# Performance work log

Hardware: AMD Instinct MI355X
Metric: run time of the kernel (lower is better)

The kernel has to match this reference:

```python
import jax, jax.numpy as jnp
import numpy as np

UP = jnp.array([0.0, 1.0, 0.0], dtype=jnp.float32)
LEASH = 15.0


def q_inv(q):
    return jnp.concatenate([-q[..., :3], q[..., 3:]], axis=-1)


def q_mul(q1, q2):
    x1, y1, z1, w1 = q1[..., 0], q1[..., 1], q1[..., 2], q1[..., 3]
    x2, y2, z2, w2 = q2[..., 0], q2[..., 1], q2[..., 2], q2[..., 3]
    return jnp.stack([
        w1 * x2 + x1 * w2 + y1 * z2 - z1 * y2,
        w1 * y2 - x1 * z2 + y1 * w2 + z1 * x2,
        w1 * z2 + x1 * y2 - y1 * x2 + z1 * w2,
        w1 * w2 - x1 * x2 - y1 * y2 - z1 * z2], axis=-1)


def q_rot(q, v):
    qv, qw = q[..., :3], q[..., 3:]
    t = 2.0 * jnp.cross(qv, v)
    return v + qw * t + jnp.cross(qv, t)


def mat_to_quat(R):
    # Batched [E,3,3] -> [E,4] (x,y,z,w), matching the torch branch structure.
    r = lambda i, j: R[:, i, j]
    eps = 1e-12
    tr = r(0, 0) + r(1, 1) + r(2, 2)
    Sa = jnp.sqrt(jnp.maximum(tr + 1.0, eps)) * 2.0
    qa = jnp.stack([(r(2, 1) - r(1, 2)) / Sa, (r(0, 2) - r(2, 0)) / Sa,
                    (r(1, 0) - r(0, 1)) / Sa, 0.25 * Sa], -1)
    Sb = jnp.sqrt(jnp.maximum(1.0 + r(0, 0) - r(1, 1) - r(2, 2), eps)) * 2.0
    qb = jnp.stack([0.25 * Sb, (r(0, 1) + r(1, 0)) / Sb,
                    (r(0, 2) + r(2, 0)) / Sb, (r(2, 1) - r(1, 2)) / Sb], -1)
    Sc = jnp.sqrt(jnp.maximum(1.0 + r(1, 1) - r(0, 0) - r(2, 2), eps)) * 2.0
    qc = jnp.stack([(r(0, 1) + r(1, 0)) / Sc, 0.25 * Sc,
                    (r(1, 2) + r(2, 1)) / Sc, (r(0, 2) - r(2, 0)) / Sc], -1)
    Sd = jnp.sqrt(jnp.maximum(1.0 + r(2, 2) - r(0, 0) - r(1, 1), eps)) * 2.0
    qd = jnp.stack([(r(0, 2) + r(2, 0)) / Sd, (r(1, 2) + r(2, 1)) / Sd,
                    0.25 * Sd, (r(1, 0) - r(0, 1)) / Sd], -1)
    cond_b = ((r(0, 0) > r(1, 1)) & (r(0, 0) > r(2, 2)))[:, None]
    cond_c = (r(1, 1) > r(2, 2))[:, None]
    return jnp.where((tr > 0)[:, None], qa,
                     jnp.where(cond_b, qb, jnp.where(cond_c, qc, qd)))


def sfm_pose_loss(pred_t, pred_q, gt_t, gt_q, batch_counts):
    E = batch_counts.shape[0]
    N = pred_t.shape[0]
    counts = batch_counts.astype(jnp.float32)  # [E]
    seg = jnp.repeat(jnp.arange(E), batch_counts, total_repeat_length=N)  # [N]
    starts = jnp.cumsum(batch_counts) - batch_counts  # first index of each episode
    sseg = lambda x: jax.ops.segment_sum(x, seg, num_segments=E)

    # --- per-episode centering ---
    mu_p = sseg(pred_t) / counts[:, None]
    mu_g = sseg(gt_t) / counts[:, None]
    p_c = pred_t - mu_p[seg]
    g_c = gt_t - mu_g[seg]

    # degenerate episodes: too short or near-zero gt variance (unbiased var)
    g_var = sseg(jnp.sum(g_c ** 2, -1)) / (counts - 1.0)
    deg = (batch_counts < 4) | (g_var < 1e-4)  # [E]

    # --- Umeyama: batched 3x3 SVD of H = p_c^T @ g_c per episode ---
    H = sseg(p_c[:, :, None] * g_c[:, None, :])  # [E,3,3]
    H_safe = jnp.where(deg[:, None, None], jnp.diag(jnp.array([3.0, 2.0, 1.0])), H)
    U, S, Vh = jnp.linalg.svd(H_safe, full_matrices=False)
    V = jnp.swapaxes(Vh, -1, -2)
    R0 = jnp.einsum('eij,ekj->eik', V, U)  # V @ U^T
    sgn = jnp.where(jnp.linalg.det(R0) < 0, -1.0, 1.0)
    V_adj = V * jnp.stack([jnp.ones_like(sgn), jnp.ones_like(sgn), sgn], -1)[:, None, :]
    R = jnp.einsum('eij,ekj->eik', V_adj, U)  # [E,3,3]

    p_rot = jnp.einsum('nij,nj->ni', R[seg], p_c)
    denom = sseg(jnp.sum(p_c ** 2, -1))
    nom = sseg(jnp.sum(p_rot * g_c, -1))
    s = jnp.where(denom > 1e-6,
                  jnp.clip(nom / jnp.maximum(denom, 1e-6), 1e-3, 1e3), 1.0)

    # --- translation loss (per-episode mse, then mean over episodes) ---
    p_al = jnp.where(deg[seg][:, None], p_c, p_rot * s[seg][:, None])
    diff = p_al - g_c
    loss_trans = jnp.mean(sseg(jnp.sum(diff ** 2, -1)) / (counts * 3.0))

    # --- scale loss (only non-degenerate episodes) ---
    loss_scale = jnp.sum(jnp.where(deg, 0.0, jnp.log(jnp.abs(s) + 1e-6) ** 2)) / E

    # --- rotation loss ---
    q_align = mat_to_quat(R)  # [E,4]
    q0_p = pred_q[starts]
    q0_g = gt_q[starts]
    pq_deg = q_mul(q_inv(q0_p)[seg], pred_q)
    gq_deg = q_mul(q_inv(q0_g)[seg], gt_q)
    pq_ume = q_mul(q_align[seg], pred_q)
    dm = deg[seg][:, None]
    pq_al = jnp.where(dm, pq_deg, pq_ume)
    gq_al = jnp.where(dm, gq_deg, gt_q)
    dot = jnp.sum(pq_al * gq_al, -1)
    loss_rot = jnp.mean(sseg(1.0 - dot ** 2) / counts)

    # --- gravity loss ---
    up = jnp.broadcast_to(UP, pred_q.shape[:-1] + (3,))
    pu = q_rot(q_inv(pred_q), up)
    gu = q_rot(q_inv(gt_q), up)
    cos = jnp.sum(pu * gu, -1) / jnp.maximum(
        jnp.linalg.norm(pu, axis=-1) * jnp.linalg.norm(gu, axis=-1), 1e-8)
    loss_grav = jnp.mean(sseg(1.0 - cos) / counts)

    # --- frame0 leash (deadzone on first translation of each episode) ---
    mag = jnp.linalg.norm(pred_t[starts], axis=-1)
    loss_leash = jnp.mean(jnp.maximum(mag - LEASH, 0.0) ** 2)

    return jnp.stack([loss_trans, loss_rot, loss_grav, loss_leash, loss_scale])


def setup_inputs() -> dict:
    rng = np.random.default_rng(0)
    E = 4096
    counts = rng.integers(64, 449, size=E)
    counts[:8] = np.array([2, 3, 3, 2, 3, 2, 3, 3])  # exercise degenerate branch
    N = int(counts.sum())
    key = jax.random.key(0)
    k1, k2, k3, k4 = jax.random.split(key, 4)
    pred_t = jax.random.normal(k1, (N, 3), dtype=jnp.float32) * 5.0
    gt_t = jax.random.normal(k2, (N, 3), dtype=jnp.float32) * 5.0

    def rand_unit_quat(k):
        q = jax.random.normal(k, (N, 4), dtype=jnp.float32)
        return q / jnp.linalg.norm(q, axis=-1, keepdims=True)

    return {
        'pred_t': pred_t,
        'pred_q': rand_unit_quat(k3),
        'gt_t': gt_t,
        'gt_q': rand_unit_quat(k4),
        'batch_counts': jnp.asarray(counts, dtype=jnp.int32),
    }


def reference(pred_t, pred_q, gt_t, gt_q, batch_counts):
    # Returns [loss_trans, loss_rot, loss_grav, loss_leash, loss_scale]
    return sfm_pose_loss(pred_t, pred_q, gt_t, gt_q, batch_counts)
```

## Files before the change

kernel.cpp:

```cpp
#include <hip/hip_runtime.h>
#include <math.h>

__global__ void scan_kernel(const int* __restrict__ counts,
                            int* __restrict__ starts,
                            float* __restrict__ out, int E) {
    __shared__ int lds[1024];
    int tid = threadIdx.x;
    if (tid < 5) out[tid] = 0.0f;
    int base = tid * 4;
    int c0 = (base + 0 < E) ? counts[base + 0] : 0;
    int c1 = (base + 1 < E) ? counts[base + 1] : 0;
    int c2 = (base + 2 < E) ? counts[base + 2] : 0;
    int c3 = (base + 3 < E) ? counts[base + 3] : 0;
    lds[tid] = c0 + c1 + c2 + c3;
    __syncthreads();
    for (int off = 1; off < 1024; off <<= 1) {
        int v = lds[tid];
        int a = (tid >= off) ? lds[tid - off] : 0;
        __syncthreads();
        lds[tid] = v + a;
        __syncthreads();
    }
    int excl = (tid > 0) ? lds[tid - 1] : 0;
    if (base + 0 < E) starts[base + 0] = excl; excl += c0;
    if (base + 1 < E) starts[base + 1] = excl; excl += c1;
    if (base + 2 < E) starts[base + 2] = excl; excl += c2;
    if (base + 3 < E) starts[base + 3] = excl;
}

__device__ __forceinline__ float4 qmul4(float4 a, float4 b) {
    return make_float4(
        a.w*b.x + a.x*b.w + a.y*b.z - a.z*b.y,
        a.w*b.y - a.x*b.z + a.y*b.w + a.z*b.x,
        a.w*b.z + a.x*b.y - a.y*b.x + a.z*b.w,
        a.w*b.w - a.x*b.x - a.y*b.y - a.z*b.z);
}

__device__ __forceinline__ void qinv_rot_up(float4 q, float out[3]) {
    float qx = -q.x, qy = -q.y, qz = -q.z, qw = q.w;
    float tx = -2.f*qz;
    float ty = 0.f;
    float tz = 2.f*qx;
    out[0] = 0.f + qw*tx + (qy*tz - qz*ty);
    out[1] = 1.f + qw*ty + (qz*tx - qx*tz);
    out[2] = 0.f + qw*tz + (qx*ty - qy*tx);
}

__device__ __forceinline__ float wave_sum(float v) {
    v += __shfl_xor(v, 32);
    v += __shfl_xor(v, 16);
    v += __shfl_xor(v, 8);
    v += __shfl_xor(v, 4);
    v += __shfl_xor(v, 2);
    v += __shfl_xor(v, 1);
    return v;
}

#define NS 29
#define CHUNK 128
#define NCH 4

__device__ __forceinline__ void accum_point(
    int i, int ci, int start,
    const float* __restrict__ pred_t, const float4* __restrict__ pred_q,
    const float* __restrict__ gt_t,   const float4* __restrict__ gt_q,
    bool small_c, float4 q0pi, float4 q0gi, float acc[NS])
{
    int m = start + min(i, ci - 1);
    float px = pred_t[3*m+0], py = pred_t[3*m+1], pz = pred_t[3*m+2];
    float gx = gt_t[3*m+0],  gy = gt_t[3*m+1],  gz = gt_t[3*m+2];
    float4 pq = pred_q[m];
    float4 gq = gt_q[m];
    if (i < ci) {
        acc[0] += px; acc[1] += py; acc[2] += pz;
        acc[3] += gx; acc[4] += gy; acc[5] += gz;
        acc[6] += px*px + py*py + pz*pz;
        acc[7] += gx*gx + gy*gy + gz*gz;
        acc[8]  += px*gx; acc[9]  += px*gy; acc[10] += px*gz;
        acc[11] += py*gx; acc[12] += py*gy; acc[13] += py*gz;
        acc[14] += pz*gx; acc[15] += pz*gy; acc[16] += pz*gz;

        float mx =  pq.w*gq.x - pq.z*gq.y + pq.y*gq.z - pq.x*gq.w;
        float my =  pq.z*gq.x + pq.w*gq.y - pq.x*gq.z - pq.y*gq.w;
        float mz = -pq.y*gq.x + pq.x*gq.y + pq.w*gq.z - pq.z*gq.w;
        float mw =  pq.x*gq.x + pq.y*gq.y + pq.z*gq.z + pq.w*gq.w;
        acc[17] += mx*mx; acc[18] += mx*my; acc[19] += mx*mz; acc[20] += mx*mw;
        acc[21] += my*my; acc[22] += my*mz; acc[23] += my*mw;
        acc[24] += mz*mz; acc[25] += mz*mw; acc[26] += mw*mw;

        float pu[3], gu[3];
        qinv_rot_up(pq, pu);
        qinv_rot_up(gq, gu);
        float cosv = pu[0]*gu[0] + pu[1]*gu[1] + pu[2]*gu[2];
        acc[27] += 1.f - cosv;

        if (small_c) {
            float4 aa = qmul4(q0pi, pq);
            float4 bb = qmul4(q0gi, gq);
            float dd = aa.x*bb.x + aa.y*bb.y + aa.z*bb.z + aa.w*bb.w;
            acc[28] += 1.f - dd*dd;
        }
    }
}

__global__ __launch_bounds__(256) void pass1_kernel(
    const float* __restrict__ pred_t, const float4* __restrict__ pred_q,
    const float* __restrict__ gt_t,   const float4* __restrict__ gt_q,
    const int* __restrict__ counts, const int* __restrict__ starts,
    float* __restrict__ P, int E)
{
    int wv = threadIdx.x >> 6;
    int lane = threadIdx.x & 63;
    int e = blockIdx.x * 4 + wv;
    if (e >= E) return;
    int ci = counts[e];
    int ch = blockIdx.y;
    int base0 = ch * CHUNK;
    if (base0 >= ci) return;
    int start = starts[e];
    bool small_c = (ci < 4);
    float4 q0pi = make_float4(0.f,0.f,0.f,0.f), q0gi = q0pi;
    if (small_c) {
        float4 q0p = pred_q[start];
        float4 q0g = gt_q[start];
        q0pi = make_float4(-q0p.x, -q0p.y, -q0p.z, q0p.w);
        q0gi = make_float4(-q0g.x, -q0g.y, -q0g.z, q0g.w);
    }

    float acc[NS];
    #pragma unroll
    for (int k = 0; k < NS; ++k) acc[k] = 0.f;

    for (int base = base0; base < ci; base += NCH * CHUNK) {
        accum_point(base + lane,      ci, start, pred_t, pred_q, gt_t, gt_q,
                    small_c, q0pi, q0gi, acc);
        accum_point(base + 64 + lane, ci, start, pred_t, pred_q, gt_t, gt_q,
                    small_c, q0pi, q0gi, acc);
    }

    #pragma unroll
    for (int k = 0; k < NS; ++k) acc[k] = wave_sum(acc[k]);

    float outv = 0.f;
    #pragma unroll
    for (int k = 0; k < NS; ++k)
        if (lane == k) outv = acc[k];
    if (lane < 32)
        P[((size_t)ch * E + e) * 32 + lane] = outv;
}

__device__ void jacobi3f(float A[3][3], float V[3][3]) {
    V[0][0]=1.f; V[0][1]=0.f; V[0][2]=0.f;
    V[1][0]=0.f; V[1][1]=1.f; V[1][2]=0.f;
    V[2][0]=0.f; V[2][1]=0.f; V[2][2]=1.f;
    for (int sweep = 0; sweep < 6; ++sweep) {
        float off = A[0][1]*A[0][1] + A[0][2]*A[0][2] + A[1][2]*A[1][2];
        float dia = A[0][0]*A[0][0] + A[1][1]*A[1][1] + A[2][2]*A[2][2];
        if (off <= 1e-12f * (dia + 1e-30f)) break;
        for (int p = 0; p < 2; ++p) for (int q = p + 1; q < 3; ++q) {
            float apq = A[p][q];
            if (fabsf(apq) < 1e-30f) continue;
            float theta = (A[q][q] - A[p][p]) / (2.0f * apq);
            float t = ((theta >= 0.f) ? 1.f : -1.f) / (fabsf(theta) + sqrtf(theta*theta + 1.f));
            float cc = 1.f / sqrtf(t*t + 1.f);
            float ss = t * cc;
            float app = A[p][p], aqq = A[q][q];
            A[p][p] = app - t * apq;
            A[q][q] = aqq + t * apq;
            A[p][q] = 0.f; A[q][p] = 0.f;
            int r = 3 - p - q;
            float arp = A[r][p], arq = A[r][q];
            A[r][p] = cc*arp - ss*arq; A[p][r] = A[r][p];
            A[r][q] = ss*arp + cc*arq; A[q][r] = A[r][q];
            for (int i = 0; i < 3; ++i) {
                float vip = V[i][p], viq = V[i][q];
                V[i][p] = cc*vip - ss*viq;
                V[i][q] = ss*vip + cc*viq;
            }
        }
    }
}

__device__ void mat2quatf(const float R[3][3], float q[4]) {
    const float eps = 1e-12f;
    float tr = R[0][0] + R[1][1] + R[2][2];
    if (tr > 0.f) {
        float S = sqrtf(fmaxf(tr + 1.f, eps)) * 2.f;
        q[0] = (R[2][1]-R[1][2])/S; q[1] = (R[0][2]-R[2][0])/S;
        q[2] = (R[1][0]-R[0][1])/S; q[3] = 0.25f*S;
    } else if ((R[0][0] > R[1][1]) && (R[0][0] > R[2][2])) {
        float S = sqrtf(fmaxf(1.f + R[0][0] - R[1][1] - R[2][2], eps)) * 2.f;
        q[0] = 0.25f*S; q[1] = (R[0][1]+R[1][0])/S;
        q[2] = (R[0][2]+R[2][0])/S; q[3] = (R[2][1]-R[1][2])/S;
    } else if (R[1][1] > R[2][2]) {
        float S = sqrtf(fmaxf(1.f + R[1][1] - R[0][0] - R[2][2], eps)) * 2.f;
        q[0] = (R[0][1]+R[1][0])/S; q[1] = 0.25f*S;
        q[2] = (R[1][2]+R[2][1])/S; q[3] = (R[0][2]-R[2][0])/S;
    } else {
        float S = sqrtf(fmaxf(1.f + R[2][2] - R[0][0] - R[1][1], eps)) * 2.f;
        q[0] = (R[0][2]+R[2][0])/S; q[1] = (R[1][2]+R[2][1])/S;
        q[2] = 0.25f*S; q[3] = (R[1][0]-R[0][1])/S;
    }
}

__global__ __launch_bounds__(64) void finalize_kernel(
    const float* __restrict__ P, const int* __restrict__ counts,
    const int* __restrict__ starts, const float* __restrict__ pred_t,
    const float4* __restrict__ pred_q, const float4* __restrict__ gt_q,
    float* __restrict__ out, int E)
{
    int e = blockIdx.x * 64 + threadIdx.x;
    float v_trans = 0.f, v_rot = 0.f, v_grav = 0.f, v_leash = 0.f, v_scale = 0.f;
    if (e < E) {
        int ci = counts[e];
        int start = starts[e];
        float A[32];
        #pragma unroll
        for (int k = 0; k < 32; ++k) A[k] = 0.f;
        #pragma unroll
        for (int ch = 0; ch < NCH; ++ch) {
            if (ch * CHUNK < ci) {
                const float4* rp = (const float4*)(P + ((size_t)ch * E + e) * 32);
                #pragma unroll
                for (int j = 0; j < 8; ++j) {
                    float4 v = rp[j];
                    A[4*j+0] += v.x; A[4*j+1] += v.y;
                    A[4*j+2] += v.z; A[4*j+3] += v.w;
                }
            }
        }
        float c = (float)ci;
        float mu_p[3] = { A[0]/c, A[1]/c, A[2]/c };
        float mu_g[3] = { A[3]/c, A[4]/c, A[5]/c };
        float pp_c = A[6] - c*(mu_p[0]*mu_p[0]+mu_p[1]*mu_p[1]+mu_p[2]*mu_p[2]);
        float gg_c = A[7] - c*(mu_g[0]*mu_g[0]+mu_g[1]*mu_g[1]+mu_g[2]*mu_g[2]);
        float H[3][3];
        H[0][0]=A[8] -c*mu_p[0]*mu_g[0]; H[0][1]=A[9] -c*mu_p[0]*mu_g[1]; H[0][2]=A[10]-c*mu_p[0]*mu_g[2];
        H[1][0]=A[11]-c*mu_p[1]*mu_g[0]; H[1][1]=A[12]-c*mu_p[1]*mu_g[1]; H[1][2]=A[13]-c*mu_p[1]*mu_g[2];
        H[2][0]=A[14]-c*mu_p[2]*mu_g[0]; H[2][1]=A[15]-c*mu_p[2]*mu_g[1]; H[2][2]=A[16]-c*mu_p[2]*mu_g[2];
        float g_var = gg_c / (c - 1.0f);
        bool small_c = (ci < 4);
        bool deg = small_c || (g_var < 1e-4f);
        float trans, rot, scale = 0.f;
        if (deg) {
            float s28;
            if (small_c) {
                s28 = A[28];
            } else {
                float4 q0p = pred_q[start];
                float4 q0g = gt_q[start];
                float4 q0pi = make_float4(-q0p.x, -q0p.y, -q0p.z, q0p.w);
                float4 q0gi = make_float4(-q0g.x, -q0g.y, -q0g.z, q0g.w);
                float local = 0.f;
                for (int ii = 0; ii < ci; ++ii) {
                    float4 aa = qmul4(q0pi, pred_q[start + ii]);
                    float4 bb = qmul4(q0gi, gt_q[start + ii]);
                    float dd = aa.x*bb.x + aa.y*bb.y + aa.z*bb.z + aa.w*bb.w;
                    local += 1.f - dd*dd;
                }
                s28 = local;
            }
            float trH = H[0][0] + H[1][1] + H[2][2];
            trans = (pp_c - 2.f*trH + gg_c) / (c * 3.f);
            rot = s28 / c;
        } else {
            float B[3][3], V[3][3];
            for (int i = 0; i < 3; ++i)
                for (int j = 0; j < 3; ++j)
                    B[i][j] = H[0][i]*H[0][j] + H[1][i]*H[1][j] + H[2][i]*H[2][j];
            jacobi3f(B, V);
            float lam[3] = { B[0][0], B[1][1], B[2][2] };
            int idx[3] = {0, 1, 2};
            if (lam[idx[0]] < lam[idx[1]]) { int t = idx[0]; idx[0] = idx[1]; idx[1] = t; }
            if (lam[idx[0]] < lam[idx[2]]) { int t = idx[0]; idx[0] = idx[2]; idx[2] = t; }
            if (lam[idx[1]] < lam[idx[2]]) { int t = idx[1]; idx[1] = idx[2]; idx[2] = t; }
            float v1[3], v2[3], v3[3];
            for (int i = 0; i < 3; ++i) { v1[i] = V[i][idx[0]]; v2[i] = V[i][idx[1]]; v3[i] = V[i][idx[2]]; }
            float detV = v1[0]*(v2[1]*v3[2]-v2[2]*v3[1])
                       - v1[1]*(v2[0]*v3[2]-v2[2]*v3[0])
                       + v1[2]*(v2[0]*v3[1]-v2[1]*v3[0]);
            float sgnV = (detV < 0.f) ? -1.f : 1.f;
            float u1[3], u2[3], u3[3];
            for (int i = 0; i < 3; ++i) u1[i] = H[i][0]*v1[0] + H[i][1]*v1[1] + H[i][2]*v1[2];
            float n1 = fmaxf(sqrtf(u1[0]*u1[0]+u1[1]*u1[1]+u1[2]*u1[2]), 1e-30f);
            for (int i = 0; i < 3; ++i) u1[i] /= n1;
            for (int i = 0; i < 3; ++i) u2[i] = H[i][0]*v2[0] + H[i][1]*v2[1] + H[i][2]*v2[2];
            float d12 = u1[0]*u2[0]+u1[1]*u2[1]+u1[2]*u2[2];
            for (int i = 0; i < 3; ++i) u2[i] -= d12*u1[i];
            float n2 = fmaxf(sqrtf(u2[0]*u2[0]+u2[1]*u2[1]+u2[2]*u2[2]), 1e-30f);
            for (int i = 0; i < 3; ++i) u2[i] /= n2;
            u3[0] = u1[1]*u2[2] - u1[2]*u2[1];
            u3[1] = u1[2]*u2[0] - u1[0]*u2[2];
            u3[2] = u1[0]*u2[1] - u1[1]*u2[0];
            float R[3][3];
            for (int i = 0; i < 3; ++i)
                for (int k = 0; k < 3; ++k)
                    R[i][k] = v1[i]*u1[k] + v2[i]*u2[k] + sgnV*v3[i]*u3[k];
            float nom = 0.f;
            for (int k = 0; k < 3; ++k)
                for (int j = 0; j < 3; ++j)
                    nom += R[k][j] * H[j][k];
            float denom = pp_c;
            float s = 1.f;
            if (denom > 1e-6f) {
                s = nom / fmaxf(denom, 1e-6f);
                s = fminf(fmaxf(s, 1e-3f), 1e3f);
            }
            trans = (s*s*denom - 2.f*s*nom + gg_c) / (c * 3.f);
            float ls = logf(fabsf(s) + 1e-6f);
            scale = ls * ls;
            float q[4];
            mat2quatf(R, q);
            float quad = q[0]*q[0]*A[17] + q[1]*q[1]*A[21] + q[2]*q[2]*A[24] + q[3]*q[3]*A[26]
                + 2.f*(q[0]*q[1]*A[18] + q[0]*q[2]*A[19] + q[0]*q[3]*A[20]
                     + q[1]*q[2]*A[22] + q[1]*q[3]*A[23] + q[2]*q[3]*A[25]);
            rot = (c - quad) / c;
        }
        float grav = A[27] / c;
        float tx = pred_t[3*start+0], ty = pred_t[3*start+1], tz = pred_t[3*start+2];
        float mag = sqrtf(tx*tx + ty*ty + tz*tz);
        float ml = fmaxf(mag - 15.f, 0.f);
        float Ed = (float)E;
        v_trans = trans / Ed;
        v_rot   = rot / Ed;
        v_grav  = grav / Ed;
        v_leash = (ml * ml) / Ed;
        v_scale = scale / Ed;
    }
    float vals[5] = { v_trans, v_rot, v_grav, v_leash, v_scale };
    #pragma unroll
    for (int k = 0; k < 5; ++k) {
        float v = wave_sum(vals[k]);
        if (threadIdx.x == 0) atomicAdd(out + k, v);
    }
}

extern "C" void kernel_launch(void* const* d_in, const int* in_sizes, int n_in,
                              void* d_out, int out_size, void* d_ws, size_t ws_size,
                              hipStream_t stream) {
    const float*  pred_t = (const float*)d_in[0];
    const float4* pred_q = (const float4*)d_in[1];
    const float*  gt_t   = (const float*)d_in[2];
    const float4* gt_q   = (const float4*)d_in[3];
    const int*    counts = (const int*)d_in[4];
    int E = in_sizes[4];

    int* starts = (int*)d_ws;
    size_t off = ((size_t)E * sizeof(int) + 255) & ~(size_t)255;
    float* P = (float*)((char*)d_ws + off);

    scan_kernel<<<1, 1024, 0, stream>>>(counts, starts, (float*)d_out, E);
    dim3 g1((E + 3) / 4, NCH);
    pass1_kernel<<<g1, 256, 0, stream>>>(pred_t, pred_q, gt_t, gt_q,
                                         counts, starts, P, E);
    finalize_kernel<<<(E + 63) / 64, 64, 0, stream>>>(P, counts, starts, pred_t,
                                                      pred_q, gt_q, (float*)d_out, E);
}
```

Baseline: 129.7 us.

## Use shuffle-based scan and two waves per episode with four points per lane

The block scan now uses wave shuffle prefix sums plus a small cross-wave pass instead of a barrier-heavy 1024-step LDS scan. Pass1 changes from four 128-point chunks per episode over a 2D grid to two waves per episode, each covering 256 contiguous points with four consecutive points per lane, and all loads are issued before the accumulation. The finalize step now sums two partials per episode instead of four. This aims to cut barrier cost, raise memory-level parallelism and halve the partial traffic. The price is less coalesced strided access per lane and fewer waves per episode.

```diff
diff --git a/kernel.cpp b/kernel.cpp
--- a/kernel.cpp
+++ b/kernel.cpp
@@ -1,27 +1,42 @@
 #include <hip/hip_runtime.h>
 #include <math.h>
+
+#define NS 29
+#define WPTS 256
 
 __global__ void scan_kernel(const int* __restrict__ counts,
                             int* __restrict__ starts,
                             float* __restrict__ out, int E) {
-    __shared__ int lds[1024];
+    __shared__ int wtot[16];
     int tid = threadIdx.x;
+    int lane = tid & 63, wv = tid >> 6;
     if (tid < 5) out[tid] = 0.0f;
     int base = tid * 4;
     int c0 = (base + 0 < E) ? counts[base + 0] : 0;
     int c1 = (base + 1 < E) ? counts[base + 1] : 0;
     int c2 = (base + 2 < E) ? counts[base + 2] : 0;
     int c3 = (base + 3 < E) ? counts[base + 3] : 0;
-    lds[tid] = c0 + c1 + c2 + c3;
+    int s = c0 + c1 + c2 + c3;
+    int incl = s;
+    #pragma unroll
+    for (int d = 1; d < 64; d <<= 1) {
+        int t = __shfl_up(incl, d);
+        if (lane >= d) incl += t;
+    }
+    if (lane == 63) wtot[wv] = incl;
     __syncthreads();
-    for (int off = 1; off < 1024; off <<= 1) {
-        int v = lds[tid];
-        int a = (tid >= off) ? lds[tid - off] : 0;
-        __syncthreads();
-        lds[tid] = v + a;
-        __syncthreads();
-    }
-    int excl = (tid > 0) ? lds[tid - 1] : 0;
+    if (wv == 0) {
+        int v = (lane < 16) ? wtot[lane] : 0;
+        int iv = v;
+        #pragma unroll
+        for (int d = 1; d < 16; d <<= 1) {
+            int t = __shfl_up(iv, d);
+            if (lane >= d) iv += t;
+        }
+        if (lane < 16) wtot[lane] = iv - v;
+    }
+    __syncthreads();
+    int excl = wtot[wv] + (incl - s);
     if (base + 0 < E) starts[base + 0] = excl; excl += c0;
     if (base + 1 < E) starts[base + 1] = excl; excl += c1;
     if (base + 2 < E) starts[base + 2] = excl; excl += c2;
@@ -56,50 +71,39 @@
     return v;
 }
 
-#define NS 29
-#define CHUNK 128
-#define NCH 4
-
-__device__ __forceinline__ void accum_point(
-    int i, int ci, int start,
-    const float* __restrict__ pred_t, const float4* __restrict__ pred_q,
-    const float* __restrict__ gt_t,   const float4* __restrict__ gt_q,
-    bool small_c, float4 q0pi, float4 q0gi, float acc[NS])
+__device__ __forceinline__ void accum_pt(
+    bool val, bool small_c,
+    float px, float py, float pz, float gx, float gy, float gz,
+    float4 pq, float4 gq, float4 q0pi, float4 q0gi, float acc[NS])
 {
-    int m = start + min(i, ci - 1);
-    float px = pred_t[3*m+0], py = pred_t[3*m+1], pz = pred_t[3*m+2];
-    float gx = gt_t[3*m+0],  gy = gt_t[3*m+1],  gz = gt_t[3*m+2];
-    float4 pq = pred_q[m];
-    float4 gq = gt_q[m];
-    if (i < ci) {
-        acc[0] += px; acc[1] += py; acc[2] += pz;
-        acc[3] += gx; acc[4] += gy; acc[5] += gz;
-        acc[6] += px*px + py*py + pz*pz;
-        acc[7] += gx*gx + gy*gy + gz*gz;
-        acc[8]  += px*gx; acc[9]  += px*gy; acc[10] += px*gz;
-        acc[11] += py*gx; acc[12] += py*gy; acc[13] += py*gz;
-        acc[14] += pz*gx; acc[15] += pz*gy; acc[16] += pz*gz;
-
-        float mx =  pq.w*gq.x - pq.z*gq.y + pq.y*gq.z - pq.x*gq.w;
-        float my =  pq.z*gq.x + pq.w*gq.y - pq.x*gq.z - pq.y*gq.w;
-        float mz = -pq.y*gq.x + pq.x*gq.y + pq.w*gq.z - pq.z*gq.w;
-        float mw =  pq.x*gq.x + pq.y*gq.y + pq.z*gq.z + pq.w*gq.w;
-        acc[17] += mx*mx; acc[18] += mx*my; acc[19] += mx*mz; acc[20] += mx*mw;
-        acc[21] += my*my; acc[22] += my*mz; acc[23] += my*mw;
-        acc[24] += mz*mz; acc[25] += mz*mw; acc[26] += mw*mw;
-
-        float pu[3], gu[3];
-        qinv_rot_up(pq, pu);
-        qinv_rot_up(gq, gu);
-        float cosv = pu[0]*gu[0] + pu[1]*gu[1] + pu[2]*gu[2];
-        acc[27] += 1.f - cosv;
-
-        if (small_c) {
-            float4 aa = qmul4(q0pi, pq);
-            float4 bb = qmul4(q0gi, gq);
-            float dd = aa.x*bb.x + aa.y*bb.y + aa.z*bb.z + aa.w*bb.w;
-            acc[28] += 1.f - dd*dd;
-        }
+    if (!val) return;
+    acc[0] += px; acc[1] += py; acc[2] += pz;
+    acc[3] += gx; acc[4] += gy; acc[5] += gz;
+    acc[6] += px*px + py*py + pz*pz;
+    acc[7] += gx*gx + gy*gy + gz*gz;
+    acc[8]  += px*gx; acc[9]  += px*gy; acc[10] += px*gz;
+    acc[11] += py*gx; acc[12] += py*gy; acc[13] += py*gz;
+    acc[14] += pz*gx; acc[15] += pz*gy; acc[16] += pz*gz;
+
+    float mx =  pq.w*gq.x - pq.z*gq.y + pq.y*gq.z - pq.x*gq.w;
+    float my =  pq.z*gq.x + pq.w*gq.y - pq.x*gq.z - pq.y*gq.w;
+    float mz = -pq.y*gq.x + pq.x*gq.y + pq.w*gq.z - pq.z*gq.w;
+    float mw =  pq.x*gq.x + pq.y*gq.y + pq.z*gq.z + pq.w*gq.w;
+    acc[17] += mx*mx; acc[18] += mx*my; acc[19] += mx*mz; acc[20] += mx*mw;
+    acc[21] += my*my; acc[22] += my*mz; acc[23] += my*mw;
+    acc[24] += mz*mz; acc[25] += mz*mw; acc[26] += mw*mw;
+
+    float pu[3], gu[3];
+    qinv_rot_up(pq, pu);
+    qinv_rot_up(gq, gu);
+    float cosv = pu[0]*gu[0] + pu[1]*gu[1] + pu[2]*gu[2];
+    acc[27] += 1.f - cosv;
+
+    if (small_c) {
+        float4 aa = qmul4(q0pi, pq);
+        float4 bb = qmul4(q0gi, gq);
+        float dd = aa.x*bb.x + aa.y*bb.y + aa.z*bb.z + aa.w*bb.w;
+        acc[28] += 1.f - dd*dd;
     }
 }
 
@@ -111,12 +115,12 @@
 {
     int wv = threadIdx.x >> 6;
     int lane = threadIdx.x & 63;
-    int e = blockIdx.x * 4 + wv;
+    int W = blockIdx.x * 4 + wv;
+    int e = W >> 1;
+    int w = W & 1;
     if (e >= E) return;
     int ci = counts[e];
-    int ch = blockIdx.y;
-    int base0 = ch * CHUNK;
-    if (base0 >= ci) return;
+    if (w * WPTS >= ci) return;
     int start = starts[e];
     bool small_c = (ci < 4);
     float4 q0pi = make_float4(0.f,0.f,0.f,0.f), q0gi = q0pi;
@@ -131,11 +135,28 @@
     #pragma unroll
     for (int k = 0; k < NS; ++k) acc[k] = 0.f;
 
-    for (int base = base0; base < ci; base += NCH * CHUNK) {
-        accum_point(base + lane,      ci, start, pred_t, pred_q, gt_t, gt_q,
-                    small_c, q0pi, q0gi, acc);
-        accum_point(base + 64 + lane, ci, start, pred_t, pred_q, gt_t, gt_q,
-                    small_c, q0pi, q0gi, acc);
+    for (int ib = w * WPTS; ib < ci; ib += 2 * WPTS) {
+        int i0 = ib + 4 * lane;
+        int m0 = start + min(i0 + 0, ci - 1);
+        int m1 = start + min(i0 + 1, ci - 1);
+        int m2 = start + min(i0 + 2, ci - 1);
+        int m3 = start + min(i0 + 3, ci - 1);
+
+        float px0 = pred_t[3*m0+0], py0 = pred_t[3*m0+1], pz0 = pred_t[3*m0+2];
+        float px1 = pred_t[3*m1+0], py1 = pred_t[3*m1+1], pz1 = pred_t[3*m1+2];
+        float px2 = pred_t[3*m2+0], py2 = pred_t[3*m2+1], pz2 = pred_t[3*m2+2];
+        float px3 = pred_t[3*m3+0], py3 = pred_t[3*m3+1], pz3 = pred_t[3*m3+2];
+        float gx0 = gt_t[3*m0+0],  gy0 = gt_t[3*m0+1],  gz0 = gt_t[3*m0+2];
+        float gx1 = gt_t[3*m1+0],  gy1 = gt_t[3*m1+1],  gz1 = gt_t[3*m1+2];
+        float gx2 = gt_t[3*m2+0],  gy2 = gt_t[3*m2+1],  gz2 = gt_t[3*m2+2];
+        float gx3 = gt_t[3*m3+0],  gy3 = gt_t[3*m3+1],  gz3 = gt_t[3*m3+2];
+        float4 pq0 = pred_q[m0], pq1 = pred_q[m1], pq2 = pred_q[m2], pq3 = pred_q[m3];
+        float4 gq0 = gt_q[m0],   gq1 = gt_q[m1],   gq2 = gt_q[m2],   gq3 = gt_q[m3];
+
+        accum_pt(i0 + 0 < ci, small_c, px0,py0,pz0, gx0,gy0,gz0, pq0, gq0, q0pi, q0gi, acc);
+        accum_pt(i0 + 1 < ci, small_c, px1,py1,pz1, gx1,gy1,gz1, pq1, gq1, q0pi, q0gi, acc);
+        accum_pt(i0 + 2 < ci, small_c, px2,py2,pz2, gx2,gy2,gz2, pq2, gq2, q0pi, q0gi, acc);
+        accum_pt(i0 + 3 < ci, small_c, px3,py3,pz3, gx3,gy3,gz3, pq3, gq3, q0pi, q0gi, acc);
     }
 
     #pragma unroll
@@ -146,7 +167,7 @@
     for (int k = 0; k < NS; ++k)
         if (lane == k) outv = acc[k];
     if (lane < 32)
-        P[((size_t)ch * E + e) * 32 + lane] = outv;
+        P[((size_t)w * E + e) * 32 + lane] = outv;
 }
 
 __device__ void jacobi3f(float A[3][3], float V[3][3]) {
@@ -218,8 +239,8 @@
         #pragma unroll
         for (int k = 0; k < 32; ++k) A[k] = 0.f;
         #pragma unroll
-        for (int ch = 0; ch < NCH; ++ch) {
-            if (ch * CHUNK < ci) {
+        for (int ch = 0; ch < 2; ++ch) {
+            if (ch * WPTS < ci) {
                 const float4* rp = (const float4*)(P + ((size_t)ch * E + e) * 32);
                 #pragma unroll
                 for (int j = 0; j < 8; ++j) {
@@ -350,9 +371,9 @@
     float* P = (float*)((char*)d_ws + off);
 
     scan_kernel<<<1, 1024, 0, stream>>>(counts, starts, (float*)d_out, E);
-    dim3 g1((E + 3) / 4, NCH);
-    pass1_kernel<<<g1, 256, 0, stream>>>(pred_t, pred_q, gt_t, gt_q,
-                                         counts, starts, P, E);
+    int nblk = (2 * E + 3) / 4;
+    pass1_kernel<<<nblk, 256, 0, stream>>>(pred_t, pred_q, gt_t, gt_q,
+                                           counts, starts, P, E);
     finalize_kernel<<<(E + 63) / 64, 64, 0, stream>>>(P, counts, starts, pred_t,
                                                       pred_q, gt_q, (float*)d_out, E);
 }
```

Result: faster. 121.0 us (-6.7%).
